# Kernel optimization log

Measured on AMD Instinct MI355X. Metric: run time of the kernel, lower is better.

Reference implementation:

```python
import jax, jax.numpy as jnp
import numpy as np

N_NODES = 50000


def _degree_norm(src, dst, n):
    # symmetric GCN normalization with self-loops already appended
    deg = jax.ops.segment_sum(jnp.ones(src.shape[0], jnp.float32), dst, num_segments=n)
    dinv = jnp.where(deg > 0, jax.lax.rsqrt(deg), 0.0)
    return dinv[src] * dinv[dst]  # [E_full]


def _gcn_layer(x, W, b, src, dst, norm, n):
    h = x @ W                                  # [N, out]
    msgs = h[src] * norm[:, None]              # gather + scale, [E_full, out]
    out = jax.ops.segment_sum(msgs, dst, num_segments=n)
    return out + b


def setup_inputs() -> dict:
    key = jax.random.key(0)
    k1, k2, k3, k4 = jax.random.split(key, 4)
    n, e, d_in, d_out = N_NODES, 800000, 256, 128
    x = jax.random.normal(k1, (n, d_in), jnp.float32)
    edge_index = jax.random.randint(k2, (2, e), 0, n, dtype=jnp.int64)
    W1 = jax.random.normal(k3, (d_in, 2 * d_out), jnp.float32) / np.sqrt(d_in)
    b1 = jnp.zeros((2 * d_out,), jnp.float32)
    W2 = jax.random.normal(k4, (2 * d_out, d_out), jnp.float32) / np.sqrt(2 * d_out)
    b2 = jnp.zeros((d_out,), jnp.float32)
    return {"x": x, "edge_index": edge_index, "W1": W1, "b1": b1, "W2": W2, "b2": b2}


def reference(x, edge_index, W1, b1, W2, b2):
    n = x.shape[0]
    loops = jnp.arange(n, dtype=edge_index.dtype)
    src = jnp.concatenate([edge_index[0], loops])
    dst = jnp.concatenate([edge_index[1], loops])
    norm = _degree_norm(src, dst, n)
    h = jax.nn.relu(_gcn_layer(x, W1, b1, src, dst, norm, n))
    h = jax.nn.relu(_gcn_layer(h, W2, b2, src, dst, norm, n))
    return h
```

## Files before the change

### kernel.cpp

```cpp
#include <hip/hip_runtime.h>
#include <hip/hip_bf16.h>


typedef __attribute__((ext_vector_type(8))) short bf16x8;
typedef __attribute__((ext_vector_type(4))) float f32x4;

__device__ inline float bf2f(unsigned short u) {
    return __uint_as_float(((unsigned)u) << 16);
}
__device__ inline unsigned short f2bf(float f) {
    unsigned x = __float_as_uint(f);
    unsigned r = (x + 0x7fffu + ((x >> 16) & 1u)) >> 16;
    return (unsigned short)r;
}

__global__ void degree_kernel(const int* __restrict__ dst, unsigned* __restrict__ deg, int E) {
    int e = blockIdx.x * blockDim.x + threadIdx.x;
    if (e < E) atomicAdd(&deg[dst[e]], 1u);
}

__global__ void dinv_kernel(const unsigned* __restrict__ deg, float* __restrict__ dinv, int N) {
    int i = blockIdx.x * blockDim.x + threadIdx.x;
    if (i < N) dinv[i] = rsqrtf((float)(deg[i] + 1u));
}

__global__ __launch_bounds__(1024) void scan_kernel(const unsigned* __restrict__ deg,
                                                    int* __restrict__ rowptr,
                                                    int* __restrict__ cursor, int N) {
    __shared__ int wsum[16];
    __shared__ int carry_s;
    const int t = threadIdx.x, lane = t & 63, w = t >> 6;
    if (t == 0) carry_s = 0;
    __syncthreads();
    for (int base = 0; base < N; base += 1024) {
        int i = base + t;
        int v = (i < N) ? (int)deg[i] : 0;
        int x = v;
#pragma unroll
        for (int off = 1; off < 64; off <<= 1) {
            int y = __shfl_up(x, off, 64);
            if (lane >= off) x += y;
        }
        if (lane == 63) wsum[w] = x;
        __syncthreads();
        if (w == 0 && lane < 16) {
            int s = wsum[lane];
#pragma unroll
            for (int off = 1; off < 16; off <<= 1) {
                int y = __shfl_up(s, off, 16);
                if ((lane & 15) >= off) s += y;
            }
            wsum[lane] = s;
        }
        __syncthreads();
        int waveoff = (w == 0) ? 0 : wsum[w - 1];
        int incl = x + waveoff;
        int excl = incl - v;
        int c = carry_s;
        if (i < N) { rowptr[i] = c + excl; cursor[i] = c + excl; }
        __syncthreads();
        if (t == 1023) carry_s = c + incl;
        __syncthreads();
    }
    if (t == 0) rowptr[N] = carry_s;
}

__global__ __launch_bounds__(256) void fill_kernel(const int* __restrict__ src,
                                                   const int* __restrict__ dst,
                                                   const float* __restrict__ dinv,
                                                   int* __restrict__ cursor,
                                                   int* __restrict__ col,
                                                   float* __restrict__ wgt, int E) {
    int e = blockIdx.x * blockDim.x + threadIdx.x;
    if (e < E) {
        int d = dst[e];
        int s = src[e];
        int pos = atomicAdd(&cursor[d], 1);
        col[pos] = s;
        wgt[pos] = dinv[s] * dinv[d];
    }
}

__global__ __launch_bounds__(256) void convert_x_kernel(const float* __restrict__ in,
                                                        unsigned short* __restrict__ out,
                                                        long n4) {
    long i = (long)blockIdx.x * blockDim.x + threadIdx.x;
    if (i < n4) {
        float4 v = ((const float4*)in)[i];
        ushort4 o;
        o.x = f2bf(v.x); o.y = f2bf(v.y); o.z = f2bf(v.z); o.w = f2bf(v.w);
        ((ushort4*)out)[i] = o;
    }
}

__global__ __launch_bounds__(256) void convert_wt_kernel(const float* __restrict__ W,
                                                         unsigned short* __restrict__ WT,
                                                         int K, int Nw) {
    int id = blockIdx.x * blockDim.x + threadIdx.x;
    if (id < K * Nw) {
        int k = id / Nw;
        int n = id % Nw;
        WT[(long)n * K + k] = f2bf(W[id]);
    }
}

#define GBM 128
#define GBN 128
#define GBK 64
__global__ __launch_bounds__(256) void gemm_bf16(const unsigned short* __restrict__ A,
                                                 const unsigned short* __restrict__ BT,
                                                 unsigned short* __restrict__ C,
                                                 int M, int Nc, int K) {
    __shared__ __align__(16) unsigned short As[GBM * GBK];
    __shared__ __align__(16) unsigned short Bs[GBN * GBK];
    const int t = threadIdx.x;
    const int lane = t & 63;
    const int w = t >> 6;
    const int row0 = blockIdx.x * GBM;
    const int col0 = blockIdx.y * GBN;
    const int rb = (w >> 1) * 64;
    const int cb = (w & 1) * 64;

    f32x4 acc[4][4] = {};

    for (int kb = 0; kb < K; kb += GBK) {
#pragma unroll
        for (int i = 0; i < 4; i++) {
            int p = i * 256 + t;
            int row = p >> 3;
            int slot = p & 7;
            int chunk = slot ^ (row & 7);
            int grow = row0 + row;
            if (grow >= M) grow = M - 1;
            const unsigned short* src = A + (size_t)grow * K + kb + chunk * 8;
            __builtin_amdgcn_global_load_lds(
                (const __attribute__((address_space(1))) void*)src,
                (__attribute__((address_space(3))) void*)&As[p * 8], 16, 0, 0);
        }
#pragma unroll
        for (int i = 0; i < 4; i++) {
            int p = i * 256 + t;
            int row = p >> 3;
            int slot = p & 7;
            int chunk = slot ^ (row & 7);
            const unsigned short* src = BT + (size_t)(col0 + row) * K + kb + chunk * 8;
            __builtin_amdgcn_global_load_lds(
                (const __attribute__((address_space(1))) void*)src,
                (__attribute__((address_space(3))) void*)&Bs[p * 8], 16, 0, 0);
        }
        asm volatile("s_waitcnt vmcnt(0)" ::: "memory");
        __syncthreads();

#pragma unroll
        for (int ks = 0; ks < 2; ks++) {
            int kq = ks * 4 + (lane >> 4);
            int rsel = lane & 15;
            bf16x8 af[4], bfr[4];
#pragma unroll
            for (int mt = 0; mt < 4; mt++) {
                int m = rb + mt * 16 + rsel;
                int slot = kq ^ (m & 7);
                af[mt] = *(const bf16x8*)&As[m * GBK + slot * 8];
            }
#pragma unroll
            for (int nt = 0; nt < 4; nt++) {
                int n = cb + nt * 16 + rsel;
                int slot = kq ^ (n & 7);
                bfr[nt] = *(const bf16x8*)&Bs[n * GBK + slot * 8];
            }
#pragma unroll
            for (int mt = 0; mt < 4; mt++)
#pragma unroll
                for (int nt = 0; nt < 4; nt++)
                    acc[mt][nt] = __builtin_amdgcn_mfma_f32_16x16x32_bf16(
                        af[mt], bfr[nt], acc[mt][nt], 0, 0, 0);
        }
        __syncthreads();
    }

#pragma unroll
    for (int mt = 0; mt < 4; mt++) {
#pragma unroll
        for (int nt = 0; nt < 4; nt++) {
            int gcol = col0 + cb + nt * 16 + (lane & 15);
            int grow0 = row0 + rb + mt * 16 + 4 * (lane >> 4);
#pragma unroll
            for (int r = 0; r < 4; r++) {
                int g = grow0 + r;
                if (g < M) C[(size_t)g * Nc + gcol] = f2bf(acc[mt][nt][r]);
            }
        }
    }
}

template <bool OUT_BF16>
__global__ void gather_kernel(const unsigned short* __restrict__ h,
                              const int* __restrict__ rowptr,
                              const int* __restrict__ col,
                              const float* __restrict__ wgt,
                              const float* __restrict__ dinv,
                              const float* __restrict__ bias,
                              void* __restrict__ out,
                              int F) {
    const int node = blockIdx.x;
    const int f0 = 2 * threadIdx.x;
    const int beg = rowptr[node];
    const int end = rowptr[node + 1];

    float a0 = 0.f, a1 = 0.f;
    int e = beg;
    for (; e + 4 <= end; e += 4) {
        int s0 = col[e], s1 = col[e + 1], s2 = col[e + 2], s3 = col[e + 3];
        float w0 = wgt[e], w1 = wgt[e + 1], w2 = wgt[e + 2], w3 = wgt[e + 3];
        ushort2 u0 = *(const ushort2*)&h[(size_t)s0 * F + f0];
        ushort2 u1 = *(const ushort2*)&h[(size_t)s1 * F + f0];
        ushort2 u2 = *(const ushort2*)&h[(size_t)s2 * F + f0];
        ushort2 u3 = *(const ushort2*)&h[(size_t)s3 * F + f0];
        a0 += bf2f(u0.x) * w0 + bf2f(u1.x) * w1 + bf2f(u2.x) * w2 + bf2f(u3.x) * w3;
        a1 += bf2f(u0.y) * w0 + bf2f(u1.y) * w1 + bf2f(u2.y) * w2 + bf2f(u3.y) * w3;
    }
    for (; e < end; e++) {
        int s = col[e];
        float wv = wgt[e];
        ushort2 u = *(const ushort2*)&h[(size_t)s * F + f0];
        a0 += bf2f(u.x) * wv;
        a1 += bf2f(u.y) * wv;
    }
    float di = dinv[node];
    ushort2 us = *(const ushort2*)&h[(size_t)node * F + f0];
    float2 bv = *(const float2*)&bias[f0];
    float v0 = fmaxf(a0 + bf2f(us.x) * di * di + bv.x, 0.f);
    float v1 = fmaxf(a1 + bf2f(us.y) * di * di + bv.y, 0.f);
    if (OUT_BF16) {
        ushort2 o; o.x = f2bf(v0); o.y = f2bf(v1);
        *(ushort2*)&((unsigned short*)out)[(size_t)node * F + f0] = o;
    } else {
        float2 o; o.x = v0; o.y = v1;
        *(float2*)&((float*)out)[(size_t)node * F + f0] = o;
    }
}

extern "C" void kernel_launch(void* const* d_in, const int* in_sizes, int n_in,
                              void* d_out, int out_size, void* d_ws, size_t ws_size,
                              hipStream_t stream) {
    const float* x  = (const float*)d_in[0];
    const int* ei   = (const int*)d_in[1];
    const float* W1 = (const float*)d_in[2];
    const float* b1 = (const float*)d_in[3];
    const float* W2 = (const float*)d_in[4];
    const float* b2 = (const float*)d_in[5];

    const int DIN = 256;
    const int N = in_sizes[0] / DIN;
    const int E = in_sizes[1] / 2;
    const int H = in_sizes[3];
    const int DOUT = in_sizes[5];

    const int* src = ei;
    const int* dst = ei + E;

    char* ws = (char*)d_ws;
    unsigned* deg = (unsigned*)ws;                   ws += (size_t)N * 4;
    float* dinv   = (float*)ws;                      ws += (size_t)N * 4;
    int* rowptr   = (int*)ws;                        ws += (size_t)(N + 4) * 4;
    int* cursor   = (int*)ws;                        ws += (size_t)N * 4;
    int* col      = (int*)ws;                        ws += (size_t)E * 4;
    float* wgt    = (float*)ws;                      ws += (size_t)E * 4;
    unsigned short* xb  = (unsigned short*)ws;       ws += (size_t)N * DIN * 2;
    unsigned short* w1t = (unsigned short*)ws;       ws += (size_t)DIN * H * 2;
    unsigned short* w2t = (unsigned short*)ws;       ws += (size_t)H * DOUT * 2;
    unsigned short* h1b = (unsigned short*)ws;       ws += (size_t)N * H * 2;
    unsigned short* y1b = (unsigned short*)ws;       ws += (size_t)N * H * 2;
    unsigned short* h2b = xb;
    float* outp = (float*)d_out;

    hipMemsetAsync(deg, 0, (size_t)N * 4, stream);
    degree_kernel<<<(E + 255) / 256, 256, 0, stream>>>(dst, deg, E);
    dinv_kernel<<<(N + 255) / 256, 256, 0, stream>>>(deg, dinv, N);
    scan_kernel<<<1, 1024, 0, stream>>>(deg, rowptr, cursor, N);
    fill_kernel<<<(E + 255) / 256, 256, 0, stream>>>(src, dst, dinv, cursor, col, wgt, E);

    {
        long n4 = (long)N * DIN / 4;
        convert_x_kernel<<<(int)((n4 + 255) / 256), 256, 0, stream>>>(x, xb, n4);
        convert_wt_kernel<<<(DIN * H + 255) / 256, 256, 0, stream>>>(W1, w1t, DIN, H);
        convert_wt_kernel<<<(H * DOUT + 255) / 256, 256, 0, stream>>>(W2, w2t, H, DOUT);
    }

    {
        dim3 grid((N + GBM - 1) / GBM, H / GBN);
        gemm_bf16<<<grid, 256, 0, stream>>>(xb, w1t, h1b, N, H, DIN);
    }
    gather_kernel<true><<<N, H / 2, 0, stream>>>(h1b, rowptr, col, wgt, dinv, b1, y1b, H);

    {
        dim3 grid((N + GBM - 1) / GBM, DOUT / GBN);
        gemm_bf16<<<grid, 256, 0, stream>>>(y1b, w2t, h2b, N, DOUT, H);
    }
    gather_kernel<false><<<N, DOUT / 2, 0, stream>>>(h2b, rowptr, col, wgt, dinv, b2, outp, DOUT);
}
```

Measured before the change: 380.3 us.

## Map one wavefront per node in gather, widen loads, unroll edges by eight

The scan kernel now processes four degrees per thread, so the serial single-block scan needs a quarter as many iterations. The gather kernel is rewritten so each 64-lane wavefront handles one node and four nodes share a 256-thread block. Each lane loads 4 or 2 bf16 values as one wider load, and the edge loop is unrolled by eight. The goal is fewer tiny blocks, more memory-level parallelism per lane and better bandwidth in the scan and the aggregation. It adds register pressure and more code paths.

```diff
diff --git a/kernel.cpp b/kernel.cpp
--- a/kernel.cpp
+++ b/kernel.cpp
@@ -13,6 +13,8 @@
     unsigned r = (x + 0x7fffu + ((x >> 16) & 1u)) >> 16;
     return (unsigned short)r;
 }
+__device__ inline float bflo(unsigned u) { return __uint_as_float(u << 16); }
+__device__ inline float bfhi(unsigned u) { return __uint_as_float(u & 0xffff0000u); }
 
 __global__ void degree_kernel(const int* __restrict__ dst, unsigned* __restrict__ deg, int E) {
     int e = blockIdx.x * blockDim.x + threadIdx.x;
@@ -32,10 +34,16 @@
     const int t = threadIdx.x, lane = t & 63, w = t >> 6;
     if (t == 0) carry_s = 0;
     __syncthreads();
-    for (int base = 0; base < N; base += 1024) {
-        int i = base + t;
-        int v = (i < N) ? (int)deg[i] : 0;
-        int x = v;
+    for (int base = 0; base < N; base += 4096) {
+        int i0 = base + t * 4;
+        int v[4];
+#pragma unroll
+        for (int j = 0; j < 4; j++) {
+            int i = i0 + j;
+            v[j] = (i < N) ? (int)deg[i] : 0;
+        }
+        int s = v[0] + v[1] + v[2] + v[3];
+        int x = s;
 #pragma unroll
         for (int off = 1; off < 64; off <<= 1) {
             int y = __shfl_up(x, off, 64);
@@ -44,22 +52,26 @@
         if (lane == 63) wsum[w] = x;
         __syncthreads();
         if (w == 0 && lane < 16) {
-            int s = wsum[lane];
+            int ss = wsum[lane];
 #pragma unroll
             for (int off = 1; off < 16; off <<= 1) {
-                int y = __shfl_up(s, off, 16);
-                if ((lane & 15) >= off) s += y;
-            }
-            wsum[lane] = s;
+                int y = __shfl_up(ss, off, 16);
+                if ((lane & 15) >= off) ss += y;
+            }
+            wsum[lane] = ss;
         }
         __syncthreads();
         int waveoff = (w == 0) ? 0 : wsum[w - 1];
-        int incl = x + waveoff;
-        int excl = incl - v;
         int c = carry_s;
-        if (i < N) { rowptr[i] = c + excl; cursor[i] = c + excl; }
-        __syncthreads();
-        if (t == 1023) carry_s = c + incl;
+        int run = c + waveoff + (x - s);
+#pragma unroll
+        for (int j = 0; j < 4; j++) {
+            int i = i0 + j;
+            if (i < N) { rowptr[i] = run; cursor[i] = run; }
+            run += v[j];
+        }
+        __syncthreads();
+        if (t == 1023) carry_s = c + waveoff + x;
         __syncthreads();
     }
     if (t == 0) rowptr[N] = carry_s;
@@ -193,50 +205,133 @@
     }
 }
 
-template <bool OUT_BF16>
-__global__ void gather_kernel(const unsigned short* __restrict__ h,
-                              const int* __restrict__ rowptr,
-                              const int* __restrict__ col,
-                              const float* __restrict__ wgt,
-                              const float* __restrict__ dinv,
-                              const float* __restrict__ bias,
-                              void* __restrict__ out,
-                              int F) {
-    const int node = blockIdx.x;
-    const int f0 = 2 * threadIdx.x;
-    const int beg = rowptr[node];
-    const int end = rowptr[node + 1];
-
-    float a0 = 0.f, a1 = 0.f;
+template <int VPL, bool OUT_BF16>
+__global__ __launch_bounds__(256) void gather_v2(const unsigned short* __restrict__ h,
+                                                 const int* __restrict__ rowptr,
+                                                 const int* __restrict__ col,
+                                                 const float* __restrict__ wgt,
+                                                 const float* __restrict__ dinv,
+                                                 const float* __restrict__ bias,
+                                                 void* __restrict__ out,
+                                                 int N) {
+    constexpr int F = VPL * 64;
+    const int wv = threadIdx.x >> 6;
+    const int lane = threadIdx.x & 63;
+    const int node = blockIdx.x * 4 + wv;
+    if (node >= N) return;
+    const int f0 = lane * VPL;
+
+    const int beg = __builtin_amdgcn_readfirstlane(rowptr[node]);
+    const int end = __builtin_amdgcn_readfirstlane(rowptr[node + 1]);
+
+    float a[VPL];
+#pragma unroll
+    for (int k = 0; k < VPL; k++) a[k] = 0.f;
+
     int e = beg;
-    for (; e + 4 <= end; e += 4) {
-        int s0 = col[e], s1 = col[e + 1], s2 = col[e + 2], s3 = col[e + 3];
-        float w0 = wgt[e], w1 = wgt[e + 1], w2 = wgt[e + 2], w3 = wgt[e + 3];
-        ushort2 u0 = *(const ushort2*)&h[(size_t)s0 * F + f0];
-        ushort2 u1 = *(const ushort2*)&h[(size_t)s1 * F + f0];
-        ushort2 u2 = *(const ushort2*)&h[(size_t)s2 * F + f0];
-        ushort2 u3 = *(const ushort2*)&h[(size_t)s3 * F + f0];
-        a0 += bf2f(u0.x) * w0 + bf2f(u1.x) * w1 + bf2f(u2.x) * w2 + bf2f(u3.x) * w3;
-        a1 += bf2f(u0.y) * w0 + bf2f(u1.y) * w1 + bf2f(u2.y) * w2 + bf2f(u3.y) * w3;
+    for (; e + 8 <= end; e += 8) {
+        int s[8]; float wvv[8];
+#pragma unroll
+        for (int j = 0; j < 8; j++) { s[j] = col[e + j]; wvv[j] = wgt[e + j]; }
+        if (VPL == 4) {
+            uint2 u[8];
+#pragma unroll
+            for (int j = 0; j < 8; j++)
+                u[j] = *(const uint2*)&h[(size_t)s[j] * F + f0];
+#pragma unroll
+            for (int j = 0; j < 8; j++) {
+                a[0] += bflo(u[j].x) * wvv[j];
+                a[1] += bfhi(u[j].x) * wvv[j];
+                a[2] += bflo(u[j].y) * wvv[j];
+                a[3] += bfhi(u[j].y) * wvv[j];
+            }
+        } else {
+            unsigned u[8];
+#pragma unroll
+            for (int j = 0; j < 8; j++)
+                u[j] = *(const unsigned*)&h[(size_t)s[j] * F + f0];
+#pragma unroll
+            for (int j = 0; j < 8; j++) {
+                a[0] += bflo(u[j]) * wvv[j];
+                a[1] += bfhi(u[j]) * wvv[j];
+            }
+        }
+    }
+    if (e + 4 <= end) {
+        int s[4]; float wvv[4];
+#pragma unroll
+        for (int j = 0; j < 4; j++) { s[j] = col[e + j]; wvv[j] = wgt[e + j]; }
+        if (VPL == 4) {
+            uint2 u[4];
+#pragma unroll
+            for (int j = 0; j < 4; j++)
+                u[j] = *(const uint2*)&h[(size_t)s[j] * F + f0];
+#pragma unroll
+            for (int j = 0; j < 4; j++) {
+                a[0] += bflo(u[j].x) * wvv[j];
+                a[1] += bfhi(u[j].x) * wvv[j];
+                a[2] += bflo(u[j].y) * wvv[j];
+                a[3] += bfhi(u[j].y) * wvv[j];
+            }
+        } else {
+            unsigned u[4];
+#pragma unroll
+            for (int j = 0; j < 4; j++)
+                u[j] = *(const unsigned*)&h[(size_t)s[j] * F + f0];
+#pragma unroll
+            for (int j = 0; j < 4; j++) {
+                a[0] += bflo(u[j]) * wvv[j];
+                a[1] += bfhi(u[j]) * wvv[j];
+            }
+        }
+        e += 4;
     }
     for (; e < end; e++) {
         int s = col[e];
-        float wv = wgt[e];
-        ushort2 u = *(const ushort2*)&h[(size_t)s * F + f0];
-        a0 += bf2f(u.x) * wv;
-        a1 += bf2f(u.y) * wv;
-    }
+        float wvv = wgt[e];
+        if (VPL == 4) {
+            uint2 u = *(const uint2*)&h[(size_t)s * F + f0];
+            a[0] += bflo(u.x) * wvv;
+            a[1] += bfhi(u.x) * wvv;
+            a[2] += bflo(u.y) * wvv;
+            a[3] += bfhi(u.y) * wvv;
+        } else {
+            unsigned u = *(const unsigned*)&h[(size_t)s * F + f0];
+            a[0] += bflo(u) * wvv;
+            a[1] += bfhi(u) * wvv;
+        }
+    }
+
     float di = dinv[node];
-    ushort2 us = *(const ushort2*)&h[(size_t)node * F + f0];
-    float2 bv = *(const float2*)&bias[f0];
-    float v0 = fmaxf(a0 + bf2f(us.x) * di * di + bv.x, 0.f);
-    float v1 = fmaxf(a1 + bf2f(us.y) * di * di + bv.y, 0.f);
-    if (OUT_BF16) {
-        ushort2 o; o.x = f2bf(v0); o.y = f2bf(v1);
-        *(ushort2*)&((unsigned short*)out)[(size_t)node * F + f0] = o;
+    float sl = di * di;
+    if (VPL == 4) {
+        uint2 u = *(const uint2*)&h[(size_t)node * F + f0];
+        float4 bv = *(const float4*)&bias[f0];
+        float v0 = fmaxf(a[0] + bflo(u.x) * sl + bv.x, 0.f);
+        float v1 = fmaxf(a[1] + bfhi(u.x) * sl + bv.y, 0.f);
+        float v2 = fmaxf(a[2] + bflo(u.y) * sl + bv.z, 0.f);
+        float v3 = fmaxf(a[3] + bfhi(u.y) * sl + bv.w, 0.f);
+        if (OUT_BF16) {
+            ushort4 o;
+            o.x = f2bf(v0); o.y = f2bf(v1); o.z = f2bf(v2); o.w = f2bf(v3);
+            *(ushort4*)&((unsigned short*)out)[(size_t)node * F + f0] = o;
+        } else {
+            float4 o = {v0, v1, v2, v3};
+            *(float4*)&((float*)out)[(size_t)node * F + f0] = o;
+        }
     } else {
-        float2 o; o.x = v0; o.y = v1;
-        *(float2*)&((float*)out)[(size_t)node * F + f0] = o;
+        unsigned u = *(const unsigned*)&h[(size_t)node * F + f0];
+        float2 bv = *(const float2*)&bias[f0];
+        float v0 = fmaxf(a[0] + bflo(u) * sl + bv.x, 0.f);
+        float v1 = fmaxf(a[1] + bfhi(u) * sl + bv.y, 0.f);
+        if (OUT_BF16) {
+            ushort2 o;
+            o.x = f2bf(v0); o.y = f2bf(v1);
+            *(ushort2*)&((unsigned short*)out)[(size_t)node * F + f0] = o;
+        } else {
+            float2 o = {v0, v1};
+            *(float2*)&((float*)out)[(size_t)node * F + f0] = o;
+        }
     }
 }
 
@@ -291,11 +386,11 @@
         dim3 grid((N + GBM - 1) / GBM, H / GBN);
         gemm_bf16<<<grid, 256, 0, stream>>>(xb, w1t, h1b, N, H, DIN);
     }
-    gather_kernel<true><<<N, H / 2, 0, stream>>>(h1b, rowptr, col, wgt, dinv, b1, y1b, H);
+    gather_v2<4, true><<<(N + 3) / 4, 256, 0, stream>>>(h1b, rowptr, col, wgt, dinv, b1, y1b, N);
 
     {
         dim3 grid((N + GBM - 1) / GBM, DOUT / GBN);
         gemm_bf16<<<grid, 256, 0, stream>>>(y1b, w2t, h2b, N, DOUT, H);
     }
-    gather_kernel<false><<<N, DOUT / 2, 0, stream>>>(h2b, rowptr, col, wgt, dinv, b2, outp, DOUT);
-}
+    gather_v2<2, false><<<(N + 3) / 4, 256, 0, stream>>>(h2b, rowptr, col, wgt, dinv, b2, outp, N);
+}
```

Result: no change. 381.9 us (+0.4%).
